# Kernel tuning notes

Measured on AMD Instinct MI355X. Metric: run time of the kernel, lower is better.

## Reference

```python
import jax, jax.numpy as jnp
import numpy as np

B, N, D, H, K, ITERS = 32, 4096, 256, 4, 8, 3
DH = D // H
HID = 512
EPS = 1e-8
LN_EPS = 1e-5
SCALE = DH ** -0.5


def _ln(x, g, b):
    m = jnp.mean(x, axis=-1, keepdims=True)
    v = jnp.mean(jnp.square(x - m), axis=-1, keepdims=True)
    return (x - m) * jax.lax.rsqrt(v + LN_EPS) * g + b


def setup_inputs() -> dict:
    key = jax.random.key(0)
    ks = jax.random.split(key, 16)
    s = 1.0 / np.sqrt(D)
    inp = {
        "inputs": jax.random.normal(ks[0], (B, N, D), jnp.float32),
        "noise": jax.random.normal(ks[1], (B, K, D), jnp.float32),
        "slots_mu": jax.random.normal(ks[2], (1, 1, D), jnp.float32),
        "slots_logsigma": jax.random.normal(ks[3], (1, 1, D), jnp.float32) * 0.05,
        "g_in": jnp.ones((D,), jnp.float32), "b_in": jnp.zeros((D,), jnp.float32),
        "g_sl": jnp.ones((D,), jnp.float32), "b_sl": jnp.zeros((D,), jnp.float32),
        "g_ml": jnp.ones((D,), jnp.float32), "b_ml": jnp.zeros((D,), jnp.float32),
        "Wq": jax.random.normal(ks[4], (D, D), jnp.float32) * s,
        "Wk": jax.random.normal(ks[5], (D, D), jnp.float32) * s,
        "Wv": jax.random.normal(ks[6], (D, D), jnp.float32) * s,
        "Wc": jax.random.normal(ks[7], (D, D), jnp.float32) * s,
        "gru_wih": jax.random.normal(ks[8], (3 * D, D), jnp.float32) * s,
        "gru_whh": jax.random.normal(ks[9], (3 * D, D), jnp.float32) * s,
        "gru_bih": jnp.zeros((3 * D,), jnp.float32),
        "gru_bhh": jnp.zeros((3 * D,), jnp.float32),
        "W1": jax.random.normal(ks[10], (D, HID), jnp.float32) * s,
        "b1": jnp.zeros((HID,), jnp.float32),
        "W2": jax.random.normal(ks[11], (HID, D), jnp.float32) / np.sqrt(HID),
        "b2": jnp.zeros((D,), jnp.float32),
    }
    return inp


def _split(t):  # [B, n, D] -> [B, H, n, DH]
    b, n, _ = t.shape
    return t.reshape(b, n, H, DH).transpose(0, 2, 1, 3)


def reference(inputs, noise, slots_mu, slots_logsigma, g_in, b_in, g_sl, b_sl,
              g_ml, b_ml, Wq, Wk, Wv, Wc, gru_wih, gru_whh, gru_bih, gru_bhh,
              W1, b1, W2, b2):
    slots = slots_mu + jnp.exp(slots_logsigma) * noise  # [B, K, D]
    x = _ln(inputs, g_in, b_in)
    k_feat = _split(x @ Wk)  # [B, H, N, DH]
    v_feat = _split(x @ Wv)
    for _ in range(ITERS):
        slots_prev = slots
        q = _split(_ln(slots, g_sl, b_sl) @ Wq)  # [B, H, K, DH]
        dots = jnp.einsum('bhkd,bhnd->bhkn', q, k_feat) * SCALE
        attn = jax.nn.softmax(dots, axis=-2)  # competitive softmax over slots
        attn = attn / (jnp.sum(attn, axis=-1, keepdims=True) + EPS)
        upd = jnp.einsum('bhkn,bhnd->bhkd', attn, v_feat)
        upd = upd.transpose(0, 2, 1, 3).reshape(B, K, D) @ Wc  # combine heads
        # GRUCell (torch layout: rows r, z, n)
        u = upd.reshape(-1, D)
        h = slots_prev.reshape(-1, D)
        gi = u @ gru_wih.T + gru_bih
        gh = h @ gru_whh.T + gru_bhh
        r = jax.nn.sigmoid(gi[:, :D] + gh[:, :D])
        z = jax.nn.sigmoid(gi[:, D:2 * D] + gh[:, D:2 * D])
        ncand = jnp.tanh(gi[:, 2 * D:] + r * gh[:, 2 * D:])
        slots = ((1.0 - z) * ncand + z * h).reshape(B, K, D)
        slots = slots + (jax.nn.relu(_ln(slots, g_ml, b_ml) @ W1 + b1) @ W2 + b2)
    return slots
```

## Files before the change

kernel.cpp:

```cpp
#include <hip/hip_runtime.h>
#include <hip/hip_bf16.h>
#include <stdint.h>

typedef unsigned short u16;
typedef _Float16 f16;
typedef __attribute__((ext_vector_type(4))) float f32x4;
typedef __attribute__((ext_vector_type(8))) _Float16 h16x8;
typedef __attribute__((ext_vector_type(4))) _Float16 h16x4;

#define LN_EPS 1e-5f
#define ATT_EPS 1e-8f

__global__ __launch_bounds__(256) void init_slots_k(
    const float* __restrict__ noise, const float* __restrict__ mu,
    const float* __restrict__ lsig, float* __restrict__ slots)
{
  int i = blockIdx.x * 256 + threadIdx.x;
  int d = i & 255;
  slots[i] = mu[d] + __expf(lsig[d]) * noise[i];
}

__global__ __launch_bounds__(256) void prep_w_k(
    const float* __restrict__ Wk, const float* __restrict__ whh,
    f16* __restrict__ WkT16, float* __restrict__ whhT)
{
  int i = blockIdx.x * 256 + threadIdx.x;
  if (i < 65536) {
    int c = i >> 8, kd = i & 255;
    WkT16[i] = (f16)Wk[kd * 256 + c];
  }
  int d = i / 768, j = i - d * 768;
  whhT[i] = whh[j * 256 + d];
}

__global__ __launch_bounds__(256) void prep_f_k(
    const float* __restrict__ Wc, const float* __restrict__ wih,
    float* __restrict__ fihT)
{
  __shared__ float wcs[16][257];
  __shared__ float ws[32][257];
  int t = threadIdx.x;
  int d0 = blockIdx.x * 16, j0 = blockIdx.y * 32;
  for (int i = t; i < 4096; i += 256) {
    int r = i >> 8, c = i & 255;
    wcs[r][c] = Wc[(d0 + r) * 256 + c];
  }
  for (int i = t; i < 8192; i += 256) {
    int r = i >> 8, c = i & 255;
    ws[r][c] = wih[(j0 + r) * 256 + c];
  }
  __syncthreads();
  int dl = t & 15, jp = t >> 4;
  float a0 = 0.f, a1 = 0.f;
#pragma unroll 8
  for (int c = 0; c < 256; c++) {
    float wv = wcs[dl][c];
    a0 += wv * ws[jp][c];
    a1 += wv * ws[jp + 16][c];
  }
  fihT[(d0 + dl) * 768 + j0 + jp] = a0;
  fihT[(d0 + dl) * 768 + j0 + jp + 16] = a1;
}

__global__ __launch_bounds__(256) void ln_x_k(
    const float* __restrict__ inputs, const float* __restrict__ g_in,
    const float* __restrict__ b_in, f16* __restrict__ xln16)
{
  int t = threadIdx.x, w = t >> 6, l = t & 63;
  float4 gv = *(const float4*)(g_in + l * 4);
  float4 bv = *(const float4*)(b_in + l * 4);
  long row0 = (long)blockIdx.x * 64 + w * 16;
#pragma unroll 2
  for (int i = 0; i < 16; i++) {
    long r = row0 + i;
    float4 x = *(const float4*)(inputs + r * 256 + l * 4);
    float s1 = x.x + x.y + x.z + x.w;
    float s2 = x.x * x.x + x.y * x.y + x.z * x.z + x.w * x.w;
#pragma unroll
    for (int off = 1; off < 64; off <<= 1) {
      s1 += __shfl_xor(s1, off);
      s2 += __shfl_xor(s2, off);
    }
    float m = s1 * (1.f / 256.f);
    float var = s2 * (1.f / 256.f) - m * m;
    float rs = rsqrtf(var + LN_EPS);
    h16x4 o;
    o[0] = (f16)((x.x - m) * rs * gv.x + bv.x);
    o[1] = (f16)((x.y - m) * rs * gv.y + bv.y);
    o[2] = (f16)((x.z - m) * rs * gv.z + bv.z);
    o[3] = (f16)((x.w - m) * rs * gv.w + bv.w);
    *(h16x4*)(xln16 + r * 256 + l * 4) = o;
  }
}

__global__ __launch_bounds__(1024) void slot_t_k(
    const float* __restrict__ slots, const float* __restrict__ g_sl,
    const float* __restrict__ b_sl, const float* __restrict__ Wq,
    const f16* __restrict__ WkT16, f16* __restrict__ tq)
{
  __shared__ float ln[256];
  __shared__ float qs[256];
  __shared__ float part[4][256];
  __shared__ float red[8];
  int t = threadIdx.x;
  int i = blockIdx.x;
  if (t < 256) {
    float x = slots[i * 256 + t];
    float a = x, bq = x * x;
#pragma unroll
    for (int off = 32; off; off >>= 1) { a += __shfl_down(a, off); bq += __shfl_down(bq, off); }
    if ((t & 63) == 0) { red[t >> 6] = a; red[4 + (t >> 6)] = bq; }
  }
  __syncthreads();
  if (t < 256) {
    float x = slots[i * 256 + t];
    float S1 = red[0] + red[1] + red[2] + red[3];
    float S2 = red[4] + red[5] + red[6] + red[7];
    float m = S1 * (1.f / 256.f);
    float var = S2 * (1.f / 256.f) - m * m;
    float rstd = rsqrtf(var + LN_EPS);
    ln[t] = (x - m) * rstd * g_sl[t] + b_sl[t];
  }
  __syncthreads();
  int col = t & 255, ks = t >> 8;
  float acc = 0.f;
#pragma unroll 16
  for (int dd = 0; dd < 64; dd++) {
    int d = ks * 64 + dd;
    acc += ln[d] * Wq[d * 256 + col];
  }
  part[ks][col] = acc;
  __syncthreads();
  if (t < 256) qs[t] = part[0][t] + part[1][t] + part[2][t] + part[3][t];
  __syncthreads();
  int h = t >> 8, d2 = t & 255;
  float tt = 0.f;
#pragma unroll 8
  for (int dp = 0; dp < 64; dp++)
    tt += qs[h * 64 + dp] * (float)WkT16[(h * 64 + dp) * 256 + d2];
  tq[((i >> 3) * 32 + h * 8 + (i & 7)) * 256 + d2] = (f16)(tt * 0.125f);
}

__global__ __launch_bounds__(256, 2) void attn_fused_k(
    const f16* __restrict__ xln16, const f16* __restrict__ tq,
    f16* __restrict__ y_part, float* __restrict__ sums_part)
{
  __shared__ u16 xs[64 * 256];
  __shared__ u16 xsT[256 * 64];
  __shared__ u16 attT[32 * 64];
  __shared__ float asum_s[4][32];
  int b = blockIdx.x, nc = blockIdx.y, t = threadIdx.x;
  int nb = nc * 128;
  int w = t >> 6, l = t & 63;
  int lc = l & 15, lg = l >> 4;
  h16x8 tb0[8], tb1[8];
#pragma unroll
  for (int k0 = 0; k0 < 8; k0++) {
    tb0[k0] = *(const h16x8*)(tq + (b * 32 + lc) * 256 + k0 * 32 + lg * 8);
    tb1[k0] = *(const h16x8*)(tq + (b * 32 + lc + 16) * 256 + k0 * 32 + lg * 8);
  }
  f32x4 acc0[4], acc1[4];
#pragma unroll
  for (int dt = 0; dt < 4; dt++) { acc0[dt] = (f32x4){0,0,0,0}; acc1[dt] = (f32x4){0,0,0,0}; }
  float as0 = 0.f, as1 = 0.f;

  for (int sub = 0; sub < 2; sub++) {
    __syncthreads();
    {
      int nl8 = t >> 5, dchunk = t & 31;
      const f16* gp = xln16 + ((long)(b * 4096 + nb + sub * 64 + nl8 * 8)) * 256 + dchunk * 8;
      h16x8 v0 = *(const h16x8*)(gp);
      h16x8 v1 = *(const h16x8*)(gp + 256);
      h16x8 v2 = *(const h16x8*)(gp + 512);
      h16x8 v3 = *(const h16x8*)(gp + 768);
      h16x8 v4 = *(const h16x8*)(gp + 1024);
      h16x8 v5 = *(const h16x8*)(gp + 1280);
      h16x8 v6 = *(const h16x8*)(gp + 1536);
      h16x8 v7 = *(const h16x8*)(gp + 1792);
      {
        int r0 = nl8 * 8;
        *(h16x8*)((char*)xs + (r0 + 0) * 512 + ((dchunk ^ ((r0 + 0) & 31)) << 4)) = v0;
        *(h16x8*)((char*)xs + (r0 + 1) * 512 + ((dchunk ^ ((r0 + 1) & 31)) << 4)) = v1;
        *(h16x8*)((char*)xs + (r0 + 2) * 512 + ((dchunk ^ ((r0 + 2) & 31)) << 4)) = v2;
        *(h16x8*)((char*)xs + (r0 + 3) * 512 + ((dchunk ^ ((r0 + 3) & 31)) << 4)) = v3;
        *(h16x8*)((char*)xs + (r0 + 4) * 512 + ((dchunk ^ ((r0 + 4) & 31)) << 4)) = v4;
        *(h16x8*)((char*)xs + (r0 + 5) * 512 + ((dchunk ^ ((r0 + 5) & 31)) << 4)) = v5;
        *(h16x8*)((char*)xs + (r0 + 6) * 512 + ((dchunk ^ ((r0 + 6) & 31)) << 4)) = v6;
        *(h16x8*)((char*)xs + (r0 + 7) * 512 + ((dchunk ^ ((r0 + 7) & 31)) << 4)) = v7;
      }
#pragma unroll
      for (int j = 0; j < 8; j++) {
        h16x8 o;
        o[0] = v0[j]; o[1] = v1[j]; o[2] = v2[j]; o[3] = v3[j];
        o[4] = v4[j]; o[5] = v5[j]; o[6] = v6[j]; o[7] = v7[j];
        int d = dchunk * 8 + j;
        *(h16x8*)((char*)xsT + d * 128 + ((nl8 ^ j) << 4)) = o;
      }
    }
    __syncthreads();
    f32x4 D0 = {0,0,0,0}, D1 = {0,0,0,0};
    {
      int row = w * 16 + lc, sw = row & 31;
#pragma unroll
      for (int k0 = 0; k0 < 8; k0++) {
        int sd8 = k0 * 4 + lg;
        h16x8 af = *(const h16x8*)((char*)xs + row * 512 + ((sd8 ^ sw) << 4));
        D0 = __builtin_amdgcn_mfma_f32_16x16x32_f16(af, tb0[k0], D0, 0, 0, 0);
        D1 = __builtin_amdgcn_mfma_f32_16x16x32_f16(af, tb1[k0], D1, 0, 0, 0);
      }
    }
    h16x4 pk0, pk1;
#pragma unroll
    for (int r = 0; r < 4; r++) {
      float d0 = D0[r], d1 = D1[r];
      float m0 = d0, m1 = d1;
      m0 = fmaxf(m0, __shfl_xor(m0, 1)); m0 = fmaxf(m0, __shfl_xor(m0, 2)); m0 = fmaxf(m0, __shfl_xor(m0, 4));
      m1 = fmaxf(m1, __shfl_xor(m1, 1)); m1 = fmaxf(m1, __shfl_xor(m1, 2)); m1 = fmaxf(m1, __shfl_xor(m1, 4));
      float e0 = __expf(d0 - m0), e1 = __expf(d1 - m1);
      float s0 = e0, s1 = e1;
      s0 += __shfl_xor(s0, 1); s0 += __shfl_xor(s0, 2); s0 += __shfl_xor(s0, 4);
      s1 += __shfl_xor(s1, 1); s1 += __shfl_xor(s1, 2); s1 += __shfl_xor(s1, 4);
      f16 a0h = (f16)(e0 / s0), a1h = (f16)(e1 / s1);
      as0 += (float)a0h; as1 += (float)a1h;
      pk0[r] = a0h; pk1[r] = a1h;
    }
    {
      int slot = w * 2 + (lg >> 1);
      int boff = (lg & 1) * 8;
      *(h16x4*)((char*)attT + lc * 128 + ((slot ^ (lc & 7)) << 4) + boff) = pk0;
      *(h16x4*)((char*)attT + (lc + 16) * 128 + ((slot ^ (lc & 7)) << 4) + boff) = pk1;
    }
    __syncthreads();
    h16x8 A00, A01, A10, A11;
    {
      int hs0 = lc, hs1 = 16 + lc, sw = lc & 7;
      A00 = *(const h16x8*)((char*)attT + hs0 * 128 + ((lg ^ sw) << 4));
      A01 = *(const h16x8*)((char*)attT + hs0 * 128 + (((4 + lg) ^ sw) << 4));
      A10 = *(const h16x8*)((char*)attT + hs1 * 128 + ((lg ^ sw) << 4));
      A11 = *(const h16x8*)((char*)attT + hs1 * 128 + (((4 + lg) ^ sw) << 4));
    }
#pragma unroll
    for (int dt = 0; dt < 4; dt++) {
      int d = w * 64 + dt * 16 + lc;
      h16x8 B0 = *(const h16x8*)((char*)xsT + d * 128 + ((lg ^ (d & 7)) << 4));
      h16x8 B1 = *(const h16x8*)((char*)xsT + d * 128 + (((4 + lg) ^ (d & 7)) << 4));
      acc0[dt] = __builtin_amdgcn_mfma_f32_16x16x32_f16(A00, B0, acc0[dt], 0, 0, 0);
      acc0[dt] = __builtin_amdgcn_mfma_f32_16x16x32_f16(A01, B1, acc0[dt], 0, 0, 0);
      acc1[dt] = __builtin_amdgcn_mfma_f32_16x16x32_f16(A10, B0, acc1[dt], 0, 0, 0);
      acc1[dt] = __builtin_amdgcn_mfma_f32_16x16x32_f16(A11, B1, acc1[dt], 0, 0, 0);
    }
  }
  as0 += __shfl_xor(as0, 16); as0 += __shfl_xor(as0, 32);
  as1 += __shfl_xor(as1, 16); as1 += __shfl_xor(as1, 32);
  if (l < 16) { asum_s[w][l] = as0; asum_s[w][l + 16] = as1; }
  __syncthreads();
  if (t < 32)
    sums_part[(nc * 32 + b) * 32 + t] =
        asum_s[0][t] + asum_s[1][t] + asum_s[2][t] + asum_s[3][t];
  long ybase = ((long)(nc * 32 + b) * 32) * 256;
#pragma unroll
  for (int reg = 0; reg < 4; reg++) {
    int hsA = lg * 4 + reg;
#pragma unroll
    for (int dt = 0; dt < 4; dt++) {
      int d = w * 64 + dt * 16 + lc;
      y_part[ybase + hsA * 256 + d] = (f16)acc0[dt][reg];
      y_part[ybase + (16 + hsA) * 256 + d] = (f16)acc1[dt][reg];
    }
  }
}

__global__ __launch_bounds__(1024) void combine_k(
    const f16* __restrict__ y_part, const float* __restrict__ sums_part,
    float* __restrict__ slots, const float* __restrict__ Wv,
    const float* __restrict__ fihT, const float* __restrict__ whhT,
    const float* __restrict__ bih, const float* __restrict__ bhh,
    const float* __restrict__ g_ml, const float* __restrict__ b_ml,
    const float* __restrict__ W1, const float* __restrict__ b1,
    const float* __restrict__ W2, const float* __restrict__ b2,
    const float* __restrict__ g_sl, const float* __restrict__ b_sl,
    const float* __restrict__ Wq, const f16* __restrict__ WkT16,
    f16* __restrict__ tq, int cq)
{
  __shared__ float ysn[4][256];
  __shared__ float uls[256], hls[256], sns[256], lns[256];
  __shared__ float hid[512];
  __shared__ f32x4 part16[16][64];
  __shared__ f32x4 part5q[8][128];
  __shared__ float part6[4][256][7];
  __shared__ float red[8];
  int t = threadIdx.x;
  int i = blockIdx.x;
  int b = i >> 3, k = i & 7;
  {
    int j = t >> 8, d = t & 255;
    float den = ATT_EPS, yv = 0.f;
#pragma unroll 8
    for (int ncq = 0; ncq < 32; ncq++) {
      int hsrow = (ncq * 32 + b) * 32 + j * 8 + k;
      den += sums_part[hsrow];
      yv += (float)y_part[(long)hsrow * 256 + d];
    }
    ysn[j][d] = yv / den;
    if (t < 256) hls[t] = slots[i * 256 + t];
  }
  __syncthreads();
  int col = t & 255, ks = t >> 8;
  int qc = t & 63, ks16 = t >> 6;
  int col0 = qc * 4;
  const float* p16 = (const float*)part16;
  const float* p5 = (const float*)part5q;
  {
    int h = col0 >> 6;
    f32x4 acc = {0.f, 0.f, 0.f, 0.f};
#pragma unroll
    for (int dd = 0; dd < 16; dd++) {
      int d = ks16 * 16 + dd;
      float u = ysn[h][d];
      float4 wv = *(const float4*)(Wv + d * 256 + col0);
      acc[0] += u * wv.x; acc[1] += u * wv.y; acc[2] += u * wv.z; acc[3] += u * wv.w;
    }
    part16[ks16][qc] = acc;
  }
  __syncthreads();
  if (t < 256) {
    float s = 0.f;
#pragma unroll
    for (int q = 0; q < 16; q++) s += p16[q * 256 + t];
    uls[t] = s;
  }
  __syncthreads();
  {
    float a0 = 0.f, a1 = 0.f, a2 = 0.f, h0 = 0.f, h1 = 0.f, h2 = 0.f;
#pragma unroll 4
    for (int dd = 0; dd < 64; dd++) {
      int d = ks * 64 + dd;
      float u = uls[d], hh = hls[d];
      const float* fi = fihT + d * 768 + col;
      const float* wh = whhT + d * 768 + col;
      a0 += u * fi[0]; a1 += u * fi[256]; a2 += u * fi[512];
      h0 += hh * wh[0]; h1 += hh * wh[256]; h2 += hh * wh[512];
    }
    part6[ks][col][0] = a0; part6[ks][col][1] = a1; part6[ks][col][2] = a2;
    part6[ks][col][3] = h0; part6[ks][col][4] = h1; part6[ks][col][5] = h2;
  }
  __syncthreads();
  if (t < 256) {
    float gi0 = part6[0][t][0] + part6[1][t][0] + part6[2][t][0] + part6[3][t][0] + bih[t];
    float gi1 = part6[0][t][1] + part6[1][t][1] + part6[2][t][1] + part6[3][t][1] + bih[256 + t];
    float gi2 = part6[0][t][2] + part6[1][t][2] + part6[2][t][2] + part6[3][t][2] + bih[512 + t];
    float gh0 = part6[0][t][3] + part6[1][t][3] + part6[2][t][3] + part6[3][t][3] + bhh[t];
    float gh1 = part6[0][t][4] + part6[1][t][4] + part6[2][t][4] + part6[3][t][4] + bhh[256 + t];
    float gh2 = part6[0][t][5] + part6[1][t][5] + part6[2][t][5] + part6[3][t][5] + bhh[512 + t];
    float r = 1.f / (1.f + __expf(-(gi0 + gh0)));
    float z = 1.f / (1.f + __expf(-(gi1 + gh1)));
    float nc2 = tanhf(gi2 + r * gh2);
    float sn = (1.f - z) * nc2 + z * hls[t];
    sns[t] = sn;
    float a = sn, bq = sn * sn;
#pragma unroll
    for (int off = 32; off; off >>= 1) { a += __shfl_down(a, off); bq += __shfl_down(bq, off); }
    if ((t & 63) == 0) { red[t >> 6] = a; red[4 + (t >> 6)] = bq; }
  }
  __syncthreads();
  if (t < 256) {
    float S1 = red[0] + red[1] + red[2] + red[3];
    float S2 = red[4] + red[5] + red[6] + red[7];
    float mean = S1 * (1.f / 256.f);
    float var = S2 * (1.f / 256.f) - mean * mean;
    float rstd = rsqrtf(var + LN_EPS);
    lns[t] = (sns[t] - mean) * rstd * g_ml[t] + b_ml[t];
  }
  __syncthreads();
  {
    int qc5 = t & 127, ks8 = t >> 7;
    int c0 = qc5 * 4;
    f32x4 acc = {0.f, 0.f, 0.f, 0.f};
#pragma unroll
    for (int dd = 0; dd < 32; dd++) {
      int d = ks8 * 32 + dd;
      float u = lns[d];
      float4 wv = *(const float4*)(W1 + d * 512 + c0);
      acc[0] += u * wv.x; acc[1] += u * wv.y; acc[2] += u * wv.z; acc[3] += u * wv.w;
    }
    part5q[ks8][qc5] = acc;
  }
  __syncthreads();
  if (t < 512) {
    float s = 0.f;
#pragma unroll
    for (int q = 0; q < 8; q++) s += p5[q * 512 + t];
    hid[t] = fmaxf(s + b1[t], 0.f);
  }
  __syncthreads();
  {
    f32x4 acc = {0.f, 0.f, 0.f, 0.f};
#pragma unroll
    for (int dd = 0; dd < 32; dd++) {
      int d = ks16 * 32 + dd;
      float u = hid[d];
      float4 wv = *(const float4*)(W2 + d * 256 + col0);
      acc[0] += u * wv.x; acc[1] += u * wv.y; acc[2] += u * wv.z; acc[3] += u * wv.w;
    }
    part16[ks16][qc] = acc;
  }
  __syncthreads();
  float outv = 0.f;
  if (t < 256) {
    float s = 0.f;
#pragma unroll
    for (int q = 0; q < 16; q++) s += p16[q * 256 + t];
    outv = sns[t] + b2[t] + s;
    slots[i * 256 + t] = outv;
  }
  if (!cq) return;
  if (t < 256) {
    float a = outv, bq = outv * outv;
#pragma unroll
    for (int off = 32; off; off >>= 1) { a += __shfl_down(a, off); bq += __shfl_down(bq, off); }
    if ((t & 63) == 0) { red[t >> 6] = a; red[4 + (t >> 6)] = bq; }
  }
  __syncthreads();
  if (t < 256) {
    float S1 = red[0] + red[1] + red[2] + red[3];
    float S2 = red[4] + red[5] + red[6] + red[7];
    float mean = S1 * (1.f / 256.f);
    float var = S2 * (1.f / 256.f) - mean * mean;
    float rstd = rsqrtf(var + LN_EPS);
    lns[t] = (outv - mean) * rstd * g_sl[t] + b_sl[t];
  }
  __syncthreads();
  {
    f32x4 acc = {0.f, 0.f, 0.f, 0.f};
#pragma unroll
    for (int dd = 0; dd < 16; dd++) {
      int d = ks16 * 16 + dd;
      float u = lns[d];
      float4 wv = *(const float4*)(Wq + d * 256 + col0);
      acc[0] += u * wv.x; acc[1] += u * wv.y; acc[2] += u * wv.z; acc[3] += u * wv.w;
    }
    part16[ks16][qc] = acc;
  }
  __syncthreads();
  if (t < 256) {
    float s = 0.f;
#pragma unroll
    for (int q = 0; q < 16; q++) s += p16[q * 256 + t];
    uls[t] = s;
  }
  __syncthreads();
  {
    int h2 = t >> 8, d2 = t & 255;
    float tt = 0.f;
#pragma unroll 8
    for (int dp = 0; dp < 64; dp++)
      tt += uls[h2 * 64 + dp] * (float)WkT16[(h2 * 64 + dp) * 256 + d2];
    tq[(b * 32 + h2 * 8 + k) * 256 + d2] = (f16)(tt * 0.125f);
  }
}

extern "C" void kernel_launch(void* const* d_in, const int* in_sizes, int n_in,
                              void* d_out, int out_size, void* d_ws, size_t ws_size,
                              hipStream_t stream)
{
  const float* inputs = (const float*)d_in[0];
  const float* noise  = (const float*)d_in[1];
  const float* mu     = (const float*)d_in[2];
  const float* lsig   = (const float*)d_in[3];
  const float* g_in   = (const float*)d_in[4];
  const float* b_in   = (const float*)d_in[5];
  const float* g_sl   = (const float*)d_in[6];
  const float* b_sl   = (const float*)d_in[7];
  const float* g_ml   = (const float*)d_in[8];
  const float* b_ml   = (const float*)d_in[9];
  const float* Wq     = (const float*)d_in[10];
  const float* Wk     = (const float*)d_in[11];
  const float* Wv     = (const float*)d_in[12];
  const float* Wc     = (const float*)d_in[13];
  const float* wih    = (const float*)d_in[14];
  const float* whh    = (const float*)d_in[15];
  const float* bih    = (const float*)d_in[16];
  const float* bhh    = (const float*)d_in[17];
  const float* W1     = (const float*)d_in[18];
  const float* b1     = (const float*)d_in[19];
  const float* W2     = (const float*)d_in[20];
  const float* b2     = (const float*)d_in[21];

  char* ws = (char*)d_ws;
  f16*   xln16  = (f16*)(ws);
  f16*   y_part = (f16*)(ws + 67108864);
  f16*   tq     = (f16*)(ws + 83886080);
  float* slots  = (float*)(ws + 84410368);
  float* sumsp  = (float*)(ws + 84672512);
  f16*   WkT16  = (f16*)(ws + 84803584);
  float* fihT   = (float*)(ws + 84934656);
  float* whhT   = (float*)(ws + 85721088);

  init_slots_k<<<256, 256, 0, stream>>>(noise, mu, lsig, slots);
  prep_w_k<<<768, 256, 0, stream>>>(Wk, whh, WkT16, whhT);
  prep_f_k<<<dim3(16, 24), 256, 0, stream>>>(Wc, wih, fihT);
  ln_x_k<<<2048, 256, 0, stream>>>(inputs, g_in, b_in, xln16);
  slot_t_k<<<256, 1024, 0, stream>>>(slots, g_sl, b_sl, Wq, WkT16, tq);
  for (int it = 0; it < 3; ++it) {
    attn_fused_k<<<dim3(32, 32), 256, 0, stream>>>(xln16, tq, y_part, sumsp);
    combine_k<<<256, 1024, 0, stream>>>(y_part, sumsp, slots, Wv, fihT, whhT,
                                        bih, bhh, g_ml, b_ml, W1, b1, W2, b2,
                                        g_sl, b_sl, Wq, WkT16, tq, (it < 2) ? 1 : 0);
  }
  hipMemcpyAsync(d_out, slots, 65536 * sizeof(float), hipMemcpyDeviceToDevice, stream);
}
```

Baseline: 263.0 us.

## Double attention N-chunk per block and pair-interleave GRU weights for float2 loads

The attention kernel now covers 256 tokens per block instead of 128, which halves the grid and the number of partial y/sum rows that combine_k must reduce. The transposed GRU weight matrices (fihT, whhT) are stored with pairs of input dims interleaved, so the GRU matvec in combine_k can read them with float2 loads and half as many loop iterations. In exchange there are fewer attention blocks (512) to fill the GPU, which may lower occupancy and latency hiding.

```diff
diff --git a/kernel.cpp b/kernel.cpp
--- a/kernel.cpp
+++ b/kernel.cpp
@@ -29,8 +29,11 @@
     int c = i >> 8, kd = i & 255;
     WkT16[i] = (f16)Wk[kd * 256 + c];
   }
-  int d = i / 768, j = i - d * 768;
-  whhT[i] = whh[j * 256 + d];
+  if (i < 98304) {
+    int dp = i / 768, j = i - dp * 768;
+    whhT[2 * i]     = whh[j * 256 + 2 * dp];
+    whhT[2 * i + 1] = whh[j * 256 + 2 * dp + 1];
+  }
 }
 
 __global__ __launch_bounds__(256) void prep_f_k(
@@ -58,8 +61,9 @@
     a0 += wv * ws[jp][c];
     a1 += wv * ws[jp + 16][c];
   }
-  fihT[(d0 + dl) * 768 + j0 + jp] = a0;
-  fihT[(d0 + dl) * 768 + j0 + jp + 16] = a1;
+  int d = d0 + dl;
+  fihT[(((d >> 1) * 768) + (j0 + jp)) * 2 + (d & 1)] = a0;
+  fihT[(((d >> 1) * 768) + (j0 + jp + 16)) * 2 + (d & 1)] = a1;
 }
 
 __global__ __launch_bounds__(256) void ln_x_k(
@@ -150,7 +154,7 @@
   __shared__ u16 attT[32 * 64];
   __shared__ float asum_s[4][32];
   int b = blockIdx.x, nc = blockIdx.y, t = threadIdx.x;
-  int nb = nc * 128;
+  int nb = nc * 256;
   int w = t >> 6, l = t & 63;
   int lc = l & 15, lg = l >> 4;
   h16x8 tb0[8], tb1[8];
@@ -164,7 +168,7 @@
   for (int dt = 0; dt < 4; dt++) { acc0[dt] = (f32x4){0,0,0,0}; acc1[dt] = (f32x4){0,0,0,0}; }
   float as0 = 0.f, as1 = 0.f;
 
-  for (int sub = 0; sub < 2; sub++) {
+  for (int sub = 0; sub < 4; sub++) {
     __syncthreads();
     {
       int nl8 = t >> 5, dchunk = t & 31;
@@ -283,7 +287,7 @@
     f16* __restrict__ tq, int cq)
 {
   __shared__ float ysn[4][256];
-  __shared__ float uls[256], hls[256], sns[256], lns[256];
+  __shared__ __align__(16) float uls[256], hls[256], sns[256], lns[256];
   __shared__ float hid[512];
   __shared__ f32x4 part16[16][64];
   __shared__ f32x4 part5q[8][128];
@@ -296,7 +300,7 @@
     int j = t >> 8, d = t & 255;
     float den = ATT_EPS, yv = 0.f;
 #pragma unroll 8
-    for (int ncq = 0; ncq < 32; ncq++) {
+    for (int ncq = 0; ncq < 16; ncq++) {
       int hsrow = (ncq * 32 + b) * 32 + j * 8 + k;
       den += sums_part[hsrow];
       yv += (float)y_part[(long)hsrow * 256 + d];
@@ -331,15 +335,26 @@
   }
   __syncthreads();
   {
+    const float2* fi2 = (const float2*)fihT;
+    const float2* wh2 = (const float2*)whhT;
     float a0 = 0.f, a1 = 0.f, a2 = 0.f, h0 = 0.f, h1 = 0.f, h2 = 0.f;
 #pragma unroll 4
-    for (int dd = 0; dd < 64; dd++) {
-      int d = ks * 64 + dd;
-      float u = uls[d], hh = hls[d];
-      const float* fi = fihT + d * 768 + col;
-      const float* wh = whhT + d * 768 + col;
-      a0 += u * fi[0]; a1 += u * fi[256]; a2 += u * fi[512];
-      h0 += hh * wh[0]; h1 += hh * wh[256]; h2 += hh * wh[512];
+    for (int dd = 0; dd < 32; dd++) {
+      int dp = ks * 32 + dd;
+      float2 u2 = *(const float2*)&uls[2 * dp];
+      float2 e2 = *(const float2*)&hls[2 * dp];
+      float2 f0 = fi2[dp * 768 + col];
+      float2 f1 = fi2[dp * 768 + 256 + col];
+      float2 f2 = fi2[dp * 768 + 512 + col];
+      float2 w0 = wh2[dp * 768 + col];
+      float2 w1 = wh2[dp * 768 + 256 + col];
+      float2 w2 = wh2[dp * 768 + 512 + col];
+      a0 += u2.x * f0.x + u2.y * f0.y;
+      a1 += u2.x * f1.x + u2.y * f1.y;
+      a2 += u2.x * f2.x + u2.y * f2.y;
+      h0 += e2.x * w0.x + e2.y * w0.y;
+      h1 += e2.x * w1.x + e2.y * w1.y;
+      h2 += e2.x * w2.x + e2.y * w2.y;
     }
     part6[ks][col][0] = a0; part6[ks][col][1] = a1; part6[ks][col][2] = a2;
     part6[ks][col][3] = h0; part6[ks][col][4] = h1; part6[ks][col][5] = h2;
@@ -502,7 +517,7 @@
   ln_x_k<<<2048, 256, 0, stream>>>(inputs, g_in, b_in, xln16);
   slot_t_k<<<256, 1024, 0, stream>>>(slots, g_sl, b_sl, Wq, WkT16, tq);
   for (int it = 0; it < 3; ++it) {
-    attn_fused_k<<<dim3(32, 32), 256, 0, stream>>>(xln16, tq, y_part, sumsp);
+    attn_fused_k<<<dim3(32, 16), 256, 0, stream>>>(xln16, tq, y_part, sumsp);
     combine_k<<<256, 1024, 0, stream>>>(y_part, sumsp, slots, Wv, fihT, whhT,
                                         bih, bhh, g_ml, b_ml, W1, b1, W2, b2,
                                         g_sl, b_sl, Wq, WkT16, tq, (it < 2) ? 1 : 0);
```

Result: slower. 285.1 us (+8.4%).
